# Performance work log

Measured on AMD Instinct MI355X. Metric: run time of the kernel, lower is better.

The kernel has to match this reference:

```python
import jax, jax.numpy as jnp
import numpy as np
import math

N, C, H = 2048, 256, 8
D = C // H
T, R, E = 8, 12, 32768
BUCKETS = 21
SEED = 128


def _layernorm(x, g, b, eps=1e-5):
    mu = jnp.mean(x, axis=-1, keepdims=True)
    var = jnp.var(x, axis=-1, keepdims=True)
    return (x - mu) * jax.lax.rsqrt(var + eps) * g + b


def _bucketize_dt(dt, num_buckets):
    eps = 1e-06
    signed_log = jnp.sign(dt) * jnp.log1p(jnp.abs(dt) + eps)
    min_v, max_v = -5.0, 5.0
    norm = (jnp.clip(signed_log, min_v, max_v) - min_v) / (max_v - min_v + 1e-09)
    idx = jnp.floor(norm * (num_buckets - 1)).astype(jnp.int32)
    return jnp.clip(idx, 0, num_buckets - 1)


def setup_inputs() -> dict:
    key = jax.random.key(0)
    ks = jax.random.split(key, 24)
    s = 0.02
    inp = {
        'X': jax.random.normal(ks[0], (N, C), jnp.float32),
        'token_type': jax.random.randint(ks[1], (N,), 0, T, jnp.int32),
        'edge_src': jax.random.randint(ks[2], (E,), 0, N, jnp.int32),
        'edge_dst': jax.random.randint(ks[3], (E,), 0, N, jnp.int32),
        'edge_rel': jax.random.randint(ks[4], (E,), 0, R, jnp.int32),
        'time_vec': jax.random.normal(ks[5], (N,), jnp.float32),
        'seed_count': SEED,
        'Wq': jax.random.normal(ks[6], (C, C), jnp.float32) * s,
        'bq': jnp.zeros((C,), jnp.float32),
        'Wk': jax.random.normal(ks[7], (C, C), jnp.float32) * s,
        'bk': jnp.zeros((C,), jnp.float32),
        'Wv': jax.random.normal(ks[8], (C, C), jnp.float32) * s,
        'bv': jnp.zeros((C,), jnp.float32),
        'Wo': jax.random.normal(ks[9], (C, C), jnp.float32) * s,
        'bo': jnp.zeros((C,), jnp.float32),
        'ln1_g': jnp.ones((C,), jnp.float32),
        'ln1_b': jnp.zeros((C,), jnp.float32),
        'ln2_g': jnp.ones((C,), jnp.float32),
        'ln2_b': jnp.zeros((C,), jnp.float32),
        'W1': jax.random.normal(ks[10], (C, 4 * C), jnp.float32) * s,
        'b1': jnp.zeros((4 * C,), jnp.float32),
        'W2': jax.random.normal(ks[11], (4 * C, C), jnp.float32) * s,
        'b2': jnp.zeros((C,), jnp.float32),
        'adj_rel_bias': jnp.zeros((R, H), jnp.float32),
        'typepair_bias': jnp.zeros((T, T, H), jnp.float32),
        'temp_bias': jax.random.normal(ks[12], (BUCKETS, H), jnp.float32) * s,
    }
    return inp


def reference(X, token_type, edge_src, edge_dst, edge_rel, time_vec, seed_count,
              Wq, bq, Wk, bk, Wv, bv, Wo, bo,
              ln1_g, ln1_b, ln2_g, ln2_b, W1, b1, W2, b2,
              adj_rel_bias, typepair_bias, temp_bias):
    n = X.shape[0]
    h = _layernorm(X, ln1_g, ln1_b)
    q = (h @ Wq + bq).reshape(n, H, D)
    k = (h @ Wk + bk).reshape(n, H, D)
    v = (h @ Wv + bv).reshape(n, H, D)
    scores = jnp.einsum('nhd,mhd->hnm', q, k) / math.sqrt(D)  # [H, N, N]

    # structural bias, factored as [N, N, H] then transposed
    bias = typepair_bias[token_type][:, token_type]            # [N, N, H]
    bias = bias.at[edge_src, edge_dst].add(adj_rel_bias[edge_rel])
    # seed-wise temporal bias on the first seed_count rows
    dt = time_vec[None, :] - time_vec[:seed_count, None]       # [S, N]
    tb = temp_bias[_bucketize_dt(dt, BUCKETS)]                 # [S, N, H]
    bias = bias.at[:seed_count].add(tb)

    attn = jax.nn.softmax(scores + bias.transpose(2, 0, 1), axis=-1)
    o = jnp.einsum('hnm,mhd->nhd', attn, v).reshape(n, C)
    x = X + (o @ Wo + bo)

    h2 = _layernorm(x, ln2_g, ln2_b)
    f = jax.nn.gelu(h2 @ W1 + b1, approximate=False) @ W2 + b2
    return x + f
```

## Files before the change

kernel.cpp:

```cpp
#include <hip/hip_runtime.h>
#include <hip/hip_bf16.h>
#include <math.h>

#define NTOK 2048
#define CDIM 256
#define HHEADS 8
#define DHEAD 32
#define NEDGE 32768
#define NTILE 16
#define SPLITS 8
#define TPS 2

typedef __attribute__((ext_vector_type(8))) short short8;
typedef __attribute__((ext_vector_type(4))) short short4v;
typedef __attribute__((ext_vector_type(4))) float f32x4;

static __device__ inline short f2bf(float f) {
    __hip_bfloat16 h = __float2bfloat16(f);
    return *reinterpret_cast<short*>(&h);
}
static __device__ inline float bf2f(short s) {
    unsigned int u = ((unsigned int)(unsigned short)s) << 16;
    return *reinterpret_cast<float*>(&u);
}

__global__ __launch_bounds__(256) void ln4_kernel(const float* __restrict__ X,
    const float* __restrict__ g, const float* __restrict__ b, short* __restrict__ out)
{
    int t = threadIdx.x;
    int wv = t >> 6, lane = t & 63;
    int row = blockIdx.x * 4 + wv;

    float4 x = *(const float4*)&X[(size_t)row * CDIM + lane * 4];
    float s = x.x + x.y + x.z + x.w;
    #pragma unroll
    for (int off = 1; off < 64; off <<= 1) s += __shfl_xor(s, off);
    float mu = s * (1.0f / CDIM);
    float4 d = { x.x - mu, x.y - mu, x.z - mu, x.w - mu };
    float s2 = d.x * d.x + d.y * d.y + d.z * d.z + d.w * d.w;
    #pragma unroll
    for (int off = 1; off < 64; off <<= 1) s2 += __shfl_xor(s2, off);
    float rsig = rsqrtf(s2 * (1.0f / CDIM) + 1e-5f);
    float4 gg = *(const float4*)&g[lane * 4];
    float4 bb = *(const float4*)&b[lane * 4];
    short o4[4];
    o4[0] = f2bf(d.x * rsig * gg.x + bb.x);
    o4[1] = f2bf(d.y * rsig * gg.y + bb.y);
    o4[2] = f2bf(d.z * rsig * gg.z + bb.z);
    o4[3] = f2bf(d.w * rsig * gg.w + bb.w);
    *(short4v*)&out[(size_t)row * CDIM + lane * 4] = *(short4v*)o4;
}

template<int SRCF>
static __device__ inline void transpose_tile(const void* __restrict__ in_,
    short* __restrict__ out, int K, int N, int k0, int n0, int t)
{
    __shared__ float tile[64][65];
    int r0 = t >> 4, c0 = (t & 15) * 4;
    #pragma unroll
    for (int i = 0; i < 4; i++) {
        int r = r0 + i * 16;
        if (SRCF == 0) {
            const float* in = (const float*)in_;
            float4 v = *(const float4*)(in + (size_t)(k0 + r) * N + n0 + c0);
            tile[r][c0 + 0] = v.x; tile[r][c0 + 1] = v.y;
            tile[r][c0 + 2] = v.z; tile[r][c0 + 3] = v.w;
        } else {
            const short* in = (const short*)in_;
            short4v v = *(const short4v*)(in + (size_t)(k0 + r) * N + n0 + c0);
            tile[r][c0 + 0] = bf2f(v.x); tile[r][c0 + 1] = bf2f(v.y);
            tile[r][c0 + 2] = bf2f(v.z); tile[r][c0 + 3] = bf2f(v.w);
        }
    }
    __syncthreads();
    #pragma unroll
    for (int i = 0; i < 4; i++) {
        int nr = r0 + i * 16;
        short o4[4];
        #pragma unroll
        for (int j = 0; j < 4; j++) o4[j] = f2bf(tile[c0 + j][nr]);
        *(short4v*)(out + (size_t)(n0 + nr) * K + k0 + c0) = *(short4v*)o4;
    }
}

__global__ __launch_bounds__(256) void transpose_all_kernel(
    const float* __restrict__ Wq, const float* __restrict__ Wk,
    const float* __restrict__ Wv, const float* __restrict__ Wo,
    const float* __restrict__ W1, const float* __restrict__ W2,
    short* __restrict__ wt_qkv, short* __restrict__ wot,
    short* __restrict__ w1t, short* __restrict__ w2t)
{
    int b = blockIdx.x;
    const float* src; short* dst; int K, N, bx, by;
    if (b < 64) {
        int m = b >> 4, r = b & 15;
        src = (m == 0) ? Wq : (m == 1) ? Wk : (m == 2) ? Wv : Wo;
        dst = (m == 0) ? wt_qkv : (m == 1) ? wt_qkv + 256 * 256
            : (m == 2) ? wt_qkv + 512 * 256 : wot;
        K = 256; N = 256; bx = r & 3; by = r >> 2;
    } else if (b < 128) {
        int r = b - 64; src = W1; dst = w1t; K = 256; N = 1024; bx = r & 15; by = r >> 4;
    } else {
        int r = b - 128; src = W2; dst = w2t; K = 1024; N = 256; bx = r & 3; by = r >> 2;
    }
    transpose_tile<0>(src, dst, K, N, by * 64, bx * 64, threadIdx.x);
}

template<int EPI>
__global__ __launch_bounds__(256) void gemm_bf16_kernel(
    const short* __restrict__ A, const short* __restrict__ Bt,
    const float* __restrict__ bias, const float* __restrict__ resid,
    void* __restrict__ out_, int M, int N, int K)
{
    __shared__ short A_lds[64 * 40];
    __shared__ short B_lds[64 * 40];

    const int t = threadIdx.x;
    const int w = t >> 6, lane = t & 63, c = lane & 15, g = lane >> 4;
    const int row0 = blockIdx.y * 64, col0 = blockIdx.x * 64;
    const int arow = t >> 2, ak = (t & 3) * 8;

    f32x4 acc[4] = {};

    for (int k0 = 0; k0 < K; k0 += 32) {
        *(short8*)&A_lds[arow * 40 + ak] = *(const short8*)&A[(size_t)(row0 + arow) * K + k0 + ak];
        *(short8*)&B_lds[arow * 40 + ak] = *(const short8*)&Bt[(size_t)(col0 + arow) * K + k0 + ak];
        __syncthreads();
        short8 af = *(const short8*)&A_lds[(w * 16 + c) * 40 + g * 8];
        #pragma unroll
        for (int nf = 0; nf < 4; nf++) {
            short8 bf = *(const short8*)&B_lds[(nf * 16 + c) * 40 + g * 8];
            acc[nf] = __builtin_amdgcn_mfma_f32_16x16x32_bf16(af, bf, acc[nf], 0, 0, 0);
        }
        __syncthreads();
    }

    #pragma unroll
    for (int nf = 0; nf < 4; nf++) {
        #pragma unroll
        for (int reg = 0; reg < 4; reg++) {
            int row = row0 + w * 16 + g * 4 + reg;
            int col = col0 + nf * 16 + c;
            float v = acc[nf][reg] + bias[col];
            if (EPI == 2) {
                ((float*)out_)[(size_t)row * N + col] = v + resid[(size_t)row * N + col];
            } else {
                v = 0.5f * v * (1.0f + erff(v * 0.70710678118654752f));
                ((short*)out_)[(size_t)row * N + col] = f2bf(v);
            }
        }
    }
}

__global__ __launch_bounds__(256) void gemm_qkv_kernel(
    const short* __restrict__ A, const short* __restrict__ Bt,
    const float* __restrict__ bq, const float* __restrict__ bk, const float* __restrict__ bv,
    short* __restrict__ qk, short* __restrict__ vt)
{
    const int K = CDIM;
    __shared__ short A_lds[64 * 40];
    __shared__ short B_lds[64 * 40];

    const int t = threadIdx.x;
    const int w = t >> 6, lane = t & 63, c = lane & 15, g = lane >> 4;
    const int row0 = blockIdx.y * 64, col0 = blockIdx.x * 64;
    const int arow = t >> 2, ak = (t & 3) * 8;

    f32x4 acc[4] = {};

    for (int k0 = 0; k0 < K; k0 += 32) {
        *(short8*)&A_lds[arow * 40 + ak] = *(const short8*)&A[(size_t)(row0 + arow) * K + k0 + ak];
        *(short8*)&B_lds[arow * 40 + ak] = *(const short8*)&Bt[(size_t)(col0 + arow) * K + k0 + ak];
        __syncthreads();
        short8 af = *(const short8*)&A_lds[(w * 16 + c) * 40 + g * 8];
        #pragma unroll
        for (int nf = 0; nf < 4; nf++) {
            short8 bf = *(const short8*)&B_lds[(nf * 16 + c) * 40 + g * 8];
            acc[nf] = __builtin_amdgcn_mfma_f32_16x16x32_bf16(af, bf, acc[nf], 0, 0, 0);
        }
        __syncthreads();
    }

    const int region = col0 >> 8;
    const int colr0 = col0 & 255;
    const float* bias = (region == 0) ? bq : (region == 1) ? bk : bv;
    #pragma unroll
    for (int nf = 0; nf < 4; nf++) {
        #pragma unroll
        for (int reg = 0; reg < 4; reg++) {
            int row = row0 + w * 16 + g * 4 + reg;
            int col = colr0 + nf * 16 + c;
            float v = acc[nf][reg] + bias[col];
            if (region == 0) v *= 0.17677669529663687f;
            short bb = f2bf(v);
            if (region < 2) qk[(size_t)row * 512 + region * 256 + col] = bb;
            else            vt[(size_t)col * NTOK + row] = bb;
        }
    }
}

__global__ void edge_hist2_kernel(const int* __restrict__ src, const int* __restrict__ dst,
    int* __restrict__ cnt, int E)
{
    int e = blockIdx.x * blockDim.x + threadIdx.x;
    if (e < E) atomicAdd(&cnt[src[e] * NTILE + (dst[e] >> 7)], 1);
}

__global__ __launch_bounds__(256) void edge_scan2_kernel(const int* __restrict__ cnt,
    int* __restrict__ row_ptr, int* __restrict__ wcur)
{
    __shared__ int sums[256];
    int t = threadIdx.x;
    int base = t * 128;
    int s = 0;
    for (int i = 0; i < 128; i++) s += cnt[base + i];
    sums[t] = s;
    __syncthreads();
    for (int off = 1; off < 256; off <<= 1) {
        int v = (t >= off) ? sums[t - off] : 0;
        __syncthreads();
        sums[t] += v;
        __syncthreads();
    }
    int run = (t == 0) ? 0 : sums[t - 1];
    for (int i = 0; i < 128; i++) {
        row_ptr[base + i] = run;
        wcur[base + i] = run;
        run += cnt[base + i];
    }
    if (t == 255) row_ptr[NTOK * NTILE] = run;
}

__global__ void edge_scatter2_kernel(const int* __restrict__ src, const int* __restrict__ dst,
    const int* __restrict__ rel, int* __restrict__ wcur, int2* __restrict__ pairs, int E)
{
    int e = blockIdx.x * blockDim.x + threadIdx.x;
    if (e < E) {
        int d = dst[e];
        int pos = atomicAdd(&wcur[src[e] * NTILE + (d >> 7)], 1);
        pairs[pos] = make_int2(d, rel[e]);
    }
}

#define QBLK 32
#define KBLK 128

__global__ __launch_bounds__(256) void attn_mfma3_kernel(
    const short* __restrict__ qk, const short* __restrict__ vt,
    const int* __restrict__ token_type, const float* __restrict__ time_vec,
    const int* __restrict__ seed_ptr,
    const float* __restrict__ adj_rel_bias, const float* __restrict__ typepair_bias,
    const float* __restrict__ temp_bias,
    const int* __restrict__ row_ptr2, const int2* __restrict__ pairs2,
    float* __restrict__ Op_part, float2* __restrict__ ml_part)
{
    __shared__ __align__(16) short Q_lds[QBLK * 40];
    __shared__ __align__(16) short K_lds[KBLK * 40];
    __shared__ __align__(16) short Vt_lds[DHEAD * 136];
    __shared__ __align__(16) unsigned int P32[QBLK * 68];
    __shared__ unsigned int ttm8[KBLK / 4];
    __shared__ float tcol_s[KBLK];
    __shared__ float tt_h[64];
    __shared__ float temp_h[21];
    __shared__ float adj_h[12];
    __shared__ float2 ml[2][QBLK];

    const int h  = blockIdx.y;
    const int n0 = blockIdx.x * QBLK;
    const int sblk = blockIdx.z;
    const int t  = threadIdx.x;
    const int wv = t >> 6, lane = t & 63, c = lane & 15, g = lane >> 4;
    const int rowblk  = (wv & 1) * 16;
    const int halfIdx = wv >> 1;
    const int colhalf = halfIdx * 64;
    const int seed = seed_ptr[0];
    const bool blockTemporal = (n0 < seed);
    const int gt0 = sblk * TPS;

    if (t < 128) {
        int row = t >> 2, off = (t & 3) * 8;
        *(short8*)&Q_lds[row * 40 + off] =
            *(const short8*)&qk[(size_t)(n0 + row) * 512 + h * 32 + off];
    }
    if (t < 64)  tt_h[t] = typepair_bias[t * HHEADS + h];
    if (t < 21)  temp_h[t] = temp_bias[t * HHEADS + h];
    if (t < 12)  adj_h[t] = adj_rel_bias[t * HHEADS + h];

    const int nrow = n0 + rowblk + c;
    const int ttn = token_type[nrow];
    const bool rowTemporal = (nrow < seed);
    const float tn = time_vec[nrow];

    int2 rp01 = *(const int2*)&row_ptr2[nrow * NTILE + gt0];
    int  rp2  = row_ptr2[nrow * NTILE + gt0 + 2];

    const int krow = t >> 2, koff = (t & 3) * 8;
    const int vrow = t >> 4, voff = (t & 15) * 8;
    short8 kr0, kr1, vr0, vr1;
    int4 ttr; float tcr = 0.0f;

    auto LOADT = [&](int gt) {
        int m0 = gt * KBLK;
        const short* kp = &qk[(size_t)(m0 + krow) * 512 + 256 + h * 32 + koff];
        kr0 = *(const short8*)kp;
        kr1 = *(const short8*)(kp + (size_t)64 * 512);
        const short* vp = &vt[(size_t)(h * 32 + vrow) * NTOK + m0 + voff];
        vr0 = *(const short8*)vp;
        vr1 = *(const short8*)(vp + (size_t)16 * NTOK);
        if (t < 32) ttr = *(const int4*)&token_type[m0 + t * 4];
        if (blockTemporal && t < 128) tcr = time_vec[m0 + t];
    };
    auto WRITET = [&]() {
        *(short8*)&K_lds[krow * 40 + koff]        = kr0;
        *(short8*)&K_lds[(krow + 64) * 40 + koff] = kr1;
        *(short8*)&Vt_lds[vrow * 136 + voff]        = vr0;
        *(short8*)&Vt_lds[(vrow + 16) * 136 + voff] = vr1;
        if (t < 32)
            ttm8[t] = (unsigned)(ttr.x | (ttr.y << 8) | (ttr.z << 16) | (ttr.w << 24));
        if (blockTemporal && t < 128) tcol_s[t] = tcr;
    };

    float m_run = -INFINITY, l_run = 0.0f;
    f32x4 oacc[2] = {{0,0,0,0},{0,0,0,0}};
    const f32x4 zf = {0.0f, 0.0f, 0.0f, 0.0f};

    LOADT(gt0);
    WRITET();

    for (int tile = 0; tile < TPS; ++tile) {
        __syncthreads();
        if (tile + 1 < TPS) LOADT(gt0 + tile + 1);

        short8 qfrag = *(const short8*)&Q_lds[(rowblk + c) * 40 + g * 8];
        float vals[16];
        #pragma unroll
        for (int blk = 0; blk < 4; blk++) {
            short8 kf = *(const short8*)&K_lds[(colhalf + blk * 16 + c) * 40 + g * 8];
            f32x4 acc = __builtin_amdgcn_mfma_f32_16x16x32_bf16(kf, qfrag, zf, 0, 0, 0);
            #pragma unroll
            for (int reg = 0; reg < 4; reg++) vals[blk * 4 + reg] = acc[reg];
        }

        #pragma unroll
        for (int blk = 0; blk < 4; blk++) {
            unsigned w4 = ttm8[halfIdx * 16 + blk * 4 + g];
            #pragma unroll
            for (int reg = 0; reg < 4; reg++) {
                int ty = (w4 >> (8 * reg)) & 0xFF;
                vals[blk * 4 + reg] += tt_h[ttn * 8 + ty];
            }
        }
        if (rowTemporal) {
            #pragma unroll
            for (int blk = 0; blk < 4; blk++) {
                #pragma unroll
                for (int reg = 0; reg < 4; reg++) {
                    float dt = tcol_s[colhalf + blk * 16 + g * 4 + reg] - tn;
                    float ab = fabsf(dt) + 1e-6f;
                    float sg = (dt > 0.0f) ? 1.0f : ((dt < 0.0f) ? -1.0f : 0.0f);
                    float sl = sg * log1pf(ab);
                    sl = fminf(fmaxf(sl, -5.0f), 5.0f);
                    float norm = (sl + 5.0f) * (1.0f / (10.0f + 1e-9f));
                    int bidx = (int)floorf(norm * 20.0f);
                    bidx = min(max(bidx, 0), 20);
                    vals[blk * 4 + reg] += temp_h[bidx];
                }
            }
        }
        {
            int e0 = (tile == 0) ? rp01.x : rp01.y;
            int e1 = (tile == 0) ? rp01.y : rp2;
            for (int e = e0; e < e1; ++e) {
                int2 pr = pairs2[e];
                int dloc = pr.x & 127;
                if ((dloc >> 6) == halfIdx) {
                    int ml64 = dloc & 63;
                    if (((ml64 >> 2) & 3) == g) {
                        float ab = adj_h[pr.y];
                        int li = (ml64 >> 4) * 4 + (ml64 & 3);
                        #pragma unroll
                        for (int i = 0; i < 16; i++) vals[i] += (i == li) ? ab : 0.0f;
                    }
                }
            }
        }

        float tmax = vals[0];
        #pragma unroll
        for (int i = 1; i < 16; i++) tmax = fmaxf(tmax, vals[i]);
        tmax = fmaxf(tmax, __shfl_xor(tmax, 16));
        tmax = fmaxf(tmax, __shfl_xor(tmax, 32));
        float m_new = fmaxf(m_run, tmax);
        float psum = 0.0f;
        #pragma unroll
        for (int i = 0; i < 16; i++) { vals[i] = __expf(vals[i] - m_new); psum += vals[i]; }
        psum += __shfl_xor(psum, 16);
        psum += __shfl_xor(psum, 32);
        float scale = __expf(m_run - m_new);
        m_run = m_new;
        l_run = l_run * scale + psum;

        #pragma unroll
        for (int blk = 0; blk < 4; blk++) {
            #pragma unroll
            for (int r = 0; r < 2; r++) {
                unsigned lo = (unsigned short)f2bf(vals[blk * 4 + 2 * r]);
                unsigned hi = (unsigned short)f2bf(vals[blk * 4 + 2 * r + 1]);
                P32[(rowblk + c) * 68 + halfIdx * 32 + blk * 8 + g * 2 + r] = lo | (hi << 16);
            }
        }

        float scr[4];
        #pragma unroll
        for (int reg = 0; reg < 4; reg++) scr[reg] = __shfl(scale, 4 * g + reg);
        #pragma unroll
        for (int dblk = 0; dblk < 2; dblk++)
            #pragma unroll
            for (int reg = 0; reg < 4; reg++) oacc[dblk][reg] *= scr[reg];
        #pragma unroll
        for (int kc = 0; kc < 2; kc++) {
            short8 pa = *(const short8*)&P32[(rowblk + c) * 68 + halfIdx * 32 + kc * 16 + g * 4];
            #pragma unroll
            for (int dblk = 0; dblk < 2; dblk++) {
                short8 vb = *(const short8*)&Vt_lds[(dblk * 16 + c) * 136 + colhalf + kc * 32 + g * 8];
                oacc[dblk] = __builtin_amdgcn_mfma_f32_16x16x32_bf16(pa, vb, oacc[dblk], 0, 0, 0);
            }
        }

        __syncthreads();
        if (tile + 1 < TPS) WRITET();
    }

    __syncthreads();
    if (lane < 16) ml[halfIdx][rowblk + lane] = make_float2(m_run, l_run);
    __syncthreads();

    float* Op = (float*)K_lds;
    #pragma unroll
    for (int reg = 0; reg < 4; reg++) {
        int rw = rowblk + 4 * g + reg;
        float2 a0 = ml[0][rw], a1 = ml[1][rw];
        float mm = fmaxf(a0.x, a1.x);
        float wh = __expf((halfIdx == 0 ? a0.x : a1.x) - mm);
        Op[halfIdx * 32 * 36 + rw * 36 + c]      = oacc[0][reg] * wh;
        Op[halfIdx * 32 * 36 + rw * 36 + 16 + c] = oacc[1][reg] * wh;
    }
    __syncthreads();

    {
        int row = t >> 3, d0 = (t & 7) * 4;
        float2 a0 = ml[0][row], a1 = ml[1][row];
        float mm = fmaxf(a0.x, a1.x);
        float w0 = __expf(a0.x - mm), w1 = __expf(a1.x - mm);
        float lc = a0.y * w0 + a1.y * w1;
        float4 pa = *(const float4*)&Op[row * 36 + d0];
        float4 pb = *(const float4*)&Op[(32 + row) * 36 + d0];
        float4 sum;
        sum.x = pa.x + pb.x; sum.y = pa.y + pb.y;
        sum.z = pa.z + pb.z; sum.w = pa.w + pb.w;
        *(float4*)&Op_part[((size_t)sblk * NTOK + n0 + row) * CDIM + h * DHEAD + d0] = sum;
        if ((t & 7) == 0)
            ml_part[((size_t)sblk * NTOK + n0 + row) * HHEADS + h] = make_float2(mm, lc);
    }
}

__global__ __launch_bounds__(256) void attn_reduce_kernel(
    const float* __restrict__ Op_part, const float2* __restrict__ ml_part,
    short* __restrict__ o)
{
    int row = blockIdx.x;
    int t = threadIdx.x;
    int h = t >> 5, d = t & 31;

    float2 a[SPLITS];
    float mm = -INFINITY;
    #pragma unroll
    for (int s = 0; s < SPLITS; s++) {
        a[s] = ml_part[((size_t)s * NTOK + row) * HHEADS + h];
        mm = fmaxf(mm, a[s].x);
    }
    float l = 0.0f, w[SPLITS];
    #pragma unroll
    for (int s = 0; s < SPLITS; s++) { w[s] = __expf(a[s].x - mm); l += a[s].y * w[s]; }
    float inv = 1.0f / l;
    size_t idx = (size_t)row * CDIM + h * DHEAD + d;
    float acc = 0.0f;
    #pragma unroll
    for (int s = 0; s < SPLITS; s++)
        acc += w[s] * Op_part[(size_t)s * NTOK * CDIM + idx];
    o[idx] = f2bf(acc * inv);
}

extern "C" void kernel_launch(void* const* d_in, const int* in_sizes, int n_in,
                              void* d_out, int out_size, void* d_ws, size_t ws_size,
                              hipStream_t stream)
{
    (void)in_sizes; (void)n_in; (void)out_size; (void)ws_size;
    const float* X        = (const float*)d_in[0];
    const int* token_type = (const int*)d_in[1];
    const int* edge_src   = (const int*)d_in[2];
    const int* edge_dst   = (const int*)d_in[3];
    const int* edge_rel   = (const int*)d_in[4];
    const float* time_vec = (const float*)d_in[5];
    const int* seed_ptr   = (const int*)d_in[6];
    const float* Wq = (const float*)d_in[7];  const float* bq = (const float*)d_in[8];
    const float* Wk = (const float*)d_in[9];  const float* bk = (const float*)d_in[10];
    const float* Wv = (const float*)d_in[11]; const float* bv = (const float*)d_in[12];
    const float* Wo = (const float*)d_in[13]; const float* bo = (const float*)d_in[14];
    const float* ln1_g = (const float*)d_in[15]; const float* ln1_b = (const float*)d_in[16];
    const float* ln2_g = (const float*)d_in[17]; const float* ln2_b = (const float*)d_in[18];
    const float* W1 = (const float*)d_in[19]; const float* b1 = (const float*)d_in[20];
    const float* W2 = (const float*)d_in[21]; const float* b2 = (const float*)d_in[22];
    const float* adj_rel_bias  = (const float*)d_in[23];
    const float* typepair_bias = (const float*)d_in[24];
    const float* temp_bias     = (const float*)d_in[25];
    float* out = (float*)d_out;

    char* base = (char*)d_ws;
    size_t off = 0;
    auto alloc = [&](size_t bytes) { char* p = base + off; off += (bytes + 255) & ~(size_t)255; return p; };
    short* qk_bf   = (short*)alloc((size_t)NTOK * 512 * 2);
    short* vt_bf   = (short*)alloc((size_t)256 * NTOK * 2);
    short* h1_bf   = (short*)alloc((size_t)NTOK * 256 * 2);
    short* h2_bf   = (short*)alloc((size_t)NTOK * 256 * 2);
    short* o_bf    = (short*)alloc((size_t)NTOK * 256 * 2);
    short* mid_bf  = (short*)alloc((size_t)NTOK * 1024 * 2);
    float* xb      = (float*)alloc((size_t)NTOK * 256 * 4);
    short* wt_qkv  = (short*)alloc((size_t)768 * 256 * 2);
    short* wot     = (short*)alloc((size_t)256 * 256 * 2);
    short* w1t     = (short*)alloc((size_t)1024 * 256 * 2);
    short* w2t     = (short*)alloc((size_t)256 * 1024 * 2);
    int2*  pairs2  = (int2*)alloc((size_t)NEDGE * 8);
    int*   cnt2    = (int*)alloc((size_t)NTOK * NTILE * 4);
    int*   rowptr2 = (int*)alloc(((size_t)NTOK * NTILE + 1) * 4);
    int*   wcur2   = (int*)alloc((size_t)NTOK * NTILE * 4);
    float* Op_part = (float*)alloc((size_t)SPLITS * NTOK * CDIM * 4);
    float2* ml_part = (float2*)alloc((size_t)SPLITS * NTOK * HHEADS * 8);

    transpose_all_kernel<<<192, 256, 0, stream>>>(Wq, Wk, Wv, Wo, W1, W2,
                                                  wt_qkv, wot, w1t, w2t);

    ln4_kernel<<<NTOK / 4, 256, 0, stream>>>(X, ln1_g, ln1_b, h1_bf);

    gemm_qkv_kernel<<<dim3(12, 32), 256, 0, stream>>>(h1_bf, wt_qkv, bq, bk, bv, qk_bf, vt_bf);

    hipMemsetAsync(cnt2, 0, NTOK * NTILE * sizeof(int), stream);
    edge_hist2_kernel<<<NEDGE / 256, 256, 0, stream>>>(edge_src, edge_dst, cnt2, NEDGE);
    edge_scan2_kernel<<<1, 256, 0, stream>>>(cnt2, rowptr2, wcur2);
    edge_scatter2_kernel<<<NEDGE / 256, 256, 0, stream>>>(edge_src, edge_dst, edge_rel, wcur2, pairs2, NEDGE);

    attn_mfma3_kernel<<<dim3(NTOK / QBLK, HHEADS, SPLITS), 256, 0, stream>>>(
        qk_bf, vt_bf, token_type, time_vec, seed_ptr,
        adj_rel_bias, typepair_bias, temp_bias, rowptr2, pairs2, Op_part, ml_part);
    attn_reduce_kernel<<<NTOK, 256, 0, stream>>>(Op_part, ml_part, o_bf);

    gemm_bf16_kernel<2><<<dim3(4, 32), 256, 0, stream>>>(o_bf, wot, bo, X, xb, NTOK, 256, 256);

    ln4_kernel<<<NTOK / 4, 256, 0, stream>>>(xb, ln2_g, ln2_b, h2_bf);

    gemm_bf16_kernel<3><<<dim3(16, 32), 256, 0, stream>>>(h2_bf, w1t, b1, nullptr, mid_bf, NTOK, 1024, 256);
    gemm_bf16_kernel<2><<<dim3(4, 32), 256, 0, stream>>>(mid_bf, w2t, b2, xb, out, NTOK, 256, 1024);
}
```

Baseline: 172.4 us.

## Fold typepair bias into QK MFMA via extended head dimension

Builds per-head Q and K buffers padded to 64 features, where the extra Q features hold the typepair bias row for the query's token type and the extra K features hold a one-hot of the key's token type. The attention kernel then runs a second MFMA over the extra features, so the QK product already contains the typepair bias. This removes the per-element token-type unpacking and shared-memory bias lookup. In exchange it doubles K/Q load and LDS traffic, adds an MFMA per block and a setup kernel, and rounds the typepair bias to bf16.

```diff
diff --git a/kernel.cpp b/kernel.cpp
--- a/kernel.cpp
+++ b/kernel.cpp
@@ -10,6 +10,8 @@
 #define NTILE 16
 #define SPLITS 8
 #define TPS 2
+#define EXTD 64
+#define LE 72
 
 typedef __attribute__((ext_vector_type(8))) short short8;
 typedef __attribute__((ext_vector_type(4))) short short4v;
@@ -60,17 +62,10 @@
     #pragma unroll
     for (int i = 0; i < 4; i++) {
         int r = r0 + i * 16;
-        if (SRCF == 0) {
-            const float* in = (const float*)in_;
-            float4 v = *(const float4*)(in + (size_t)(k0 + r) * N + n0 + c0);
-            tile[r][c0 + 0] = v.x; tile[r][c0 + 1] = v.y;
-            tile[r][c0 + 2] = v.z; tile[r][c0 + 3] = v.w;
-        } else {
-            const short* in = (const short*)in_;
-            short4v v = *(const short4v*)(in + (size_t)(k0 + r) * N + n0 + c0);
-            tile[r][c0 + 0] = bf2f(v.x); tile[r][c0 + 1] = bf2f(v.y);
-            tile[r][c0 + 2] = bf2f(v.z); tile[r][c0 + 3] = bf2f(v.w);
-        }
+        const float* in = (const float*)in_;
+        float4 v = *(const float4*)(in + (size_t)(k0 + r) * N + n0 + c0);
+        tile[r][c0 + 0] = v.x; tile[r][c0 + 1] = v.y;
+        tile[r][c0 + 2] = v.z; tile[r][c0 + 3] = v.w;
     }
     __syncthreads();
     #pragma unroll
@@ -106,6 +101,29 @@
     transpose_tile<0>(src, dst, K, N, by * 64, bx * 64, threadIdx.x);
 }
 
+__global__ __launch_bounds__(256) void ext_build_kernel(
+    const int* __restrict__ token_type, const float* __restrict__ typepair_bias,
+    short* __restrict__ qh, short* __restrict__ kh)
+{
+    int idx = blockIdx.x * 256 + threadIdx.x;
+    int row = idx >> 3, h = idx & 7;
+    int tt = token_type[row];
+    short qe[32], ke[32];
+    #pragma unroll
+    for (int j = 0; j < 32; j++) {
+        if (j < 8) {
+            qe[j] = f2bf(typepair_bias[(tt * 8 + j) * 8 + h]);
+            ke[j] = (j == tt) ? (short)0x3F80 : (short)0;
+        } else { qe[j] = 0; ke[j] = 0; }
+    }
+    size_t base = ((size_t)h * NTOK + row) * EXTD + 32;
+    #pragma unroll
+    for (int k = 0; k < 4; k++) {
+        *(short8*)&qh[base + k * 8] = *(short8*)&qe[k * 8];
+        *(short8*)&kh[base + k * 8] = *(short8*)&ke[k * 8];
+    }
+}
+
 template<int EPI>
 __global__ __launch_bounds__(256) void gemm_bf16_kernel(
     const short* __restrict__ A, const short* __restrict__ Bt,
@@ -155,7 +173,7 @@
 __global__ __launch_bounds__(256) void gemm_qkv_kernel(
     const short* __restrict__ A, const short* __restrict__ Bt,
     const float* __restrict__ bq, const float* __restrict__ bk, const float* __restrict__ bv,
-    short* __restrict__ qk, short* __restrict__ vt)
+    short* __restrict__ qh, short* __restrict__ kh, short* __restrict__ vt)
 {
     const int K = CDIM;
     __shared__ short A_lds[64 * 40];
@@ -193,8 +211,10 @@
             float v = acc[nf][reg] + bias[col];
             if (region == 0) v *= 0.17677669529663687f;
             short bb = f2bf(v);
-            if (region < 2) qk[(size_t)row * 512 + region * 256 + col] = bb;
-            else            vt[(size_t)col * NTOK + row] = bb;
+            size_t hidx = ((size_t)(col >> 5) * NTOK + row) * EXTD + (col & 31);
+            if (region == 0)      qh[hidx] = bb;
+            else if (region == 1) kh[hidx] = bb;
+            else                  vt[(size_t)col * NTOK + row] = bb;
         }
     }
 }
@@ -246,21 +266,18 @@
 #define KBLK 128
 
 __global__ __launch_bounds__(256) void attn_mfma3_kernel(
-    const short* __restrict__ qk, const short* __restrict__ vt,
-    const int* __restrict__ token_type, const float* __restrict__ time_vec,
-    const int* __restrict__ seed_ptr,
-    const float* __restrict__ adj_rel_bias, const float* __restrict__ typepair_bias,
-    const float* __restrict__ temp_bias,
+    const short* __restrict__ qh, const short* __restrict__ kh,
+    const short* __restrict__ vt,
+    const float* __restrict__ time_vec, const int* __restrict__ seed_ptr,
+    const float* __restrict__ adj_rel_bias, const float* __restrict__ temp_bias,
     const int* __restrict__ row_ptr2, const int2* __restrict__ pairs2,
     float* __restrict__ Op_part, float2* __restrict__ ml_part)
 {
-    __shared__ __align__(16) short Q_lds[QBLK * 40];
-    __shared__ __align__(16) short K_lds[KBLK * 40];
+    __shared__ __align__(16) short Q_lds[QBLK * LE];
+    __shared__ __align__(16) short K_lds[KBLK * LE];
     __shared__ __align__(16) short Vt_lds[DHEAD * 136];
     __shared__ __align__(16) unsigned int P32[QBLK * 68];
-    __shared__ unsigned int ttm8[KBLK / 4];
     __shared__ float tcol_s[KBLK];
-    __shared__ float tt_h[64];
     __shared__ float temp_h[21];
     __shared__ float adj_h[12];
     __shared__ float2 ml[2][QBLK];
@@ -277,46 +294,45 @@
     const bool blockTemporal = (n0 < seed);
     const int gt0 = sblk * TPS;
 
-    if (t < 128) {
-        int row = t >> 2, off = (t & 3) * 8;
-        *(short8*)&Q_lds[row * 40 + off] =
-            *(const short8*)&qk[(size_t)(n0 + row) * 512 + h * 32 + off];
-    }
-    if (t < 64)  tt_h[t] = typepair_bias[t * HHEADS + h];
+    {
+        int row = t >> 3, off = (t & 7) * 8;
+        *(short8*)&Q_lds[row * LE + off] =
+            *(const short8*)&qh[((size_t)h * NTOK + n0 + row) * EXTD + off];
+    }
     if (t < 21)  temp_h[t] = temp_bias[t * HHEADS + h];
     if (t < 12)  adj_h[t] = adj_rel_bias[t * HHEADS + h];
 
     const int nrow = n0 + rowblk + c;
-    const int ttn = token_type[nrow];
     const bool rowTemporal = (nrow < seed);
     const float tn = time_vec[nrow];
 
     int2 rp01 = *(const int2*)&row_ptr2[nrow * NTILE + gt0];
     int  rp2  = row_ptr2[nrow * NTILE + gt0 + 2];
 
-    const int krow = t >> 2, koff = (t & 3) * 8;
+    const int krow = t >> 3, koff = (t & 7) * 8;
     const int vrow = t >> 4, voff = (t & 15) * 8;
-    short8 kr0, kr1, vr0, vr1;
-    int4 ttr; float tcr = 0.0f;
+    short8 kr0, kr1, kr2, kr3, vr0, vr1;
+    float tcr = 0.0f;
 
     auto LOADT = [&](int gt) {
         int m0 = gt * KBLK;
-        const short* kp = &qk[(size_t)(m0 + krow) * 512 + 256 + h * 32 + koff];
+        const short* kp = &kh[((size_t)h * NTOK + m0 + krow) * EXTD + koff];
         kr0 = *(const short8*)kp;
-        kr1 = *(const short8*)(kp + (size_t)64 * 512);
+        kr1 = *(const short8*)(kp + (size_t)32 * EXTD);
+        kr2 = *(const short8*)(kp + (size_t)64 * EXTD);
+        kr3 = *(const short8*)(kp + (size_t)96 * EXTD);
         const short* vp = &vt[(size_t)(h * 32 + vrow) * NTOK + m0 + voff];
         vr0 = *(const short8*)vp;
         vr1 = *(const short8*)(vp + (size_t)16 * NTOK);
-        if (t < 32) ttr = *(const int4*)&token_type[m0 + t * 4];
         if (blockTemporal && t < 128) tcr = time_vec[m0 + t];
     };
     auto WRITET = [&]() {
-        *(short8*)&K_lds[krow * 40 + koff]        = kr0;
-        *(short8*)&K_lds[(krow + 64) * 40 + koff] = kr1;
+        *(short8*)&K_lds[krow * LE + koff]        = kr0;
+        *(short8*)&K_lds[(krow + 32) * LE + koff] = kr1;
+        *(short8*)&K_lds[(krow + 64) * LE + koff] = kr2;
+        *(short8*)&K_lds[(krow + 96) * LE + koff] = kr3;
         *(short8*)&Vt_lds[vrow * 136 + voff]        = vr0;
         *(short8*)&Vt_lds[(vrow + 16) * 136 + voff] = vr1;
-        if (t < 32)
-            ttm8[t] = (unsigned)(ttr.x | (ttr.y << 8) | (ttr.z << 16) | (ttr.w << 24));
         if (blockTemporal && t < 128) tcol_s[t] = tcr;
     };
 
@@ -331,25 +347,20 @@
         __syncthreads();
         if (tile + 1 < TPS) LOADT(gt0 + tile + 1);
 
-        short8 qfrag = *(const short8*)&Q_lds[(rowblk + c) * 40 + g * 8];
+        short8 qlo = *(const short8*)&Q_lds[(rowblk + c) * LE + g * 8];
+        short8 qhi = *(const short8*)&Q_lds[(rowblk + c) * LE + 32 + g * 8];
         float vals[16];
         #pragma unroll
         for (int blk = 0; blk < 4; blk++) {
-            short8 kf = *(const short8*)&K_lds[(colhalf + blk * 16 + c) * 40 + g * 8];
-            f32x4 acc = __builtin_amdgcn_mfma_f32_16x16x32_bf16(kf, qfrag, zf, 0, 0, 0);
+            const short* kb = &K_lds[(colhalf + blk * 16 + c) * LE];
+            short8 klo = *(const short8*)(kb + g * 8);
+            short8 khi = *(const short8*)(kb + 32 + g * 8);
+            f32x4 acc = __builtin_amdgcn_mfma_f32_16x16x32_bf16(klo, qlo, zf, 0, 0, 0);
+            acc = __builtin_amdgcn_mfma_f32_16x16x32_bf16(khi, qhi, acc, 0, 0, 0);
             #pragma unroll
             for (int reg = 0; reg < 4; reg++) vals[blk * 4 + reg] = acc[reg];
         }
 
-        #pragma unroll
-        for (int blk = 0; blk < 4; blk++) {
-            unsigned w4 = ttm8[halfIdx * 16 + blk * 4 + g];
-            #pragma unroll
-            for (int reg = 0; reg < 4; reg++) {
-                int ty = (w4 >> (8 * reg)) & 0xFF;
-                vals[blk * 4 + reg] += tt_h[ttn * 8 + ty];
-            }
-        }
         if (rowTemporal) {
             #pragma unroll
             for (int blk = 0; blk < 4; blk++) {
@@ -519,7 +530,8 @@
     char* base = (char*)d_ws;
     size_t off = 0;
     auto alloc = [&](size_t bytes) { char* p = base + off; off += (bytes + 255) & ~(size_t)255; return p; };
-    short* qk_bf   = (short*)alloc((size_t)NTOK * 512 * 2);
+    short* qh_bf   = (short*)alloc((size_t)HHEADS * NTOK * EXTD * 2);
+    short* kh_bf   = (short*)alloc((size_t)HHEADS * NTOK * EXTD * 2);
     short* vt_bf   = (short*)alloc((size_t)256 * NTOK * 2);
     short* h1_bf   = (short*)alloc((size_t)NTOK * 256 * 2);
     short* h2_bf   = (short*)alloc((size_t)NTOK * 256 * 2);
@@ -539,10 +551,12 @@
 
     transpose_all_kernel<<<192, 256, 0, stream>>>(Wq, Wk, Wv, Wo, W1, W2,
                                                   wt_qkv, wot, w1t, w2t);
+    ext_build_kernel<<<64, 256, 0, stream>>>(token_type, typepair_bias, qh_bf, kh_bf);
 
     ln4_kernel<<<NTOK / 4, 256, 0, stream>>>(X, ln1_g, ln1_b, h1_bf);
 
-    gemm_qkv_kernel<<<dim3(12, 32), 256, 0, stream>>>(h1_bf, wt_qkv, bq, bk, bv, qk_bf, vt_bf);
+    gemm_qkv_kernel<<<dim3(12, 32), 256, 0, stream>>>(h1_bf, wt_qkv, bq, bk, bv,
+                                                      qh_bf, kh_bf, vt_bf);
 
     hipMemsetAsync(cnt2, 0, NTOK * NTILE * sizeof(int), stream);
     edge_hist2_kernel<<<NEDGE / 256, 256, 0, stream>>>(edge_src, edge_dst, cnt2, NEDGE);
@@ -550,8 +564,8 @@
     edge_scatter2_kernel<<<NEDGE / 256, 256, 0, stream>>>(edge_src, edge_dst, edge_rel, wcur2, pairs2, NEDGE);
 
     attn_mfma3_kernel<<<dim3(NTOK / QBLK, HHEADS, SPLITS), 256, 0, stream>>>(
-        qk_bf, vt_bf, token_type, time_vec, seed_ptr,
-        adj_rel_bias, typepair_bias, temp_bias, rowptr2, pairs2, Op_part, ml_part);
+        qh_bf, kh_bf, vt_bf, time_vec, seed_ptr,
+        adj_rel_bias, temp_bias, rowptr2, pairs2, Op_part, ml_part);
     attn_reduce_kernel<<<NTOK, 256, 0, stream>>>(Op_part, ml_part, o_bf);
 
     gemm_bf16_kernel<2><<<dim3(4, 32), 256, 0, stream>>>(o_bf, wot, bo, X, xb, NTOK, 256, 256);
```

After: 173.3 us. Within noise of the previous version (+0.5%).
